# Kernel optimization log

Hardware: AMD Instinct MI355X
Metric: run time of the kernel (lower is better)

## Reference

```python
import jax, jax.numpy as jnp
import numpy as np

NE = 64        # num experts
H = 1024       # hidden_size
F = 2048       # ffn_hidden_size per expert
T = 16384      # total tokens


def setup_inputs() -> dict:
    key = jax.random.key(0)
    k1, k2, k3 = jax.random.split(key, 3)
    x = jax.random.normal(k1, (T, H), jnp.float32)
    w1 = jax.random.normal(k2, (NE, F, H), jnp.float32) * 0.02
    w2 = jax.random.normal(k3, (NE, F, H), jnp.float32) * 0.02
    # ragged token counts per expert, summing exactly to T
    rng = np.random.default_rng(0)
    sizes = rng.multinomial(T, np.ones(NE) / NE)
    tokens_per_expert = jnp.asarray(sizes, jnp.int32)
    return {"x": x, "w1": w1, "w2": w2, "tokens_per_expert": tokens_per_expert}


def _grouped_gmm(x, w, sizes, trans_b=False):
    # grouped GEMM: per-expert segment of x multiplied by that expert's weight.
    # sizes are concrete host ints (group boundaries are static), so we emit
    # one GEMM per expert with static slices, matching gg.ops.gmm semantics.
    offs = np.concatenate([[0], np.cumsum(sizes)]).astype(np.int64)
    outs = []
    for e in range(len(sizes)):
        xe = x[int(offs[e]):int(offs[e + 1])]          # [n_e, k]
        we = w[e].T if trans_b else w[e]               # [k, n]
        outs.append(xe @ we)
    return jnp.concatenate(outs, axis=0)


def reference(x, w1, w2, tokens_per_expert):
    sizes = np.asarray(tokens_per_expert)
    h = _grouped_gmm(x, w1, sizes, trans_b=True)       # [T, F]
    h = jax.nn.gelu(h, approximate=False)              # torch F.gelu (exact erf)
    return _grouped_gmm(h, w2, sizes, trans_b=False)   # [T, H]
```

## Files before the change

kernel.cpp:

```cpp
#include <hip/hip_runtime.h>
#include <hip/hip_bf16.h>

#define NE 64
#define HDIM 1024
#define FDIM 2048
#define TDIM 16384

typedef __attribute__((ext_vector_type(8))) short short8;
typedef __attribute__((ext_vector_type(4))) float f32x4;
typedef unsigned short u16;
typedef unsigned int u32;

struct IC0 { static constexpr int v = 0; };
struct IC1 { static constexpr int v = 1; };
template<int W> struct WN { static constexpr int v = W; };

__device__ __forceinline__ u16 f2bf(float f) {
  return __bfloat16_as_ushort(__float2bfloat16(f));
}
__device__ __forceinline__ u32 pk2(float a, float b) {
  return (u32)f2bf(a) | ((u32)f2bf(b) << 16);
}
template<int N> __device__ __forceinline__ void waitv() {
  if constexpr (N == 2)       asm volatile("s_waitcnt vmcnt(2)" ::: "memory");
  else if constexpr (N == 4)  asm volatile("s_waitcnt vmcnt(4)" ::: "memory");
  else if constexpr (N == 8)  asm volatile("s_waitcnt vmcnt(8)" ::: "memory");
  else if constexpr (N == 10) asm volatile("s_waitcnt vmcnt(10)" ::: "memory");
}
__device__ __forceinline__ void waitl() {
  asm volatile("s_waitcnt lgkmcnt(0)" ::: "memory");
}

__global__ void k_prep(const int* __restrict__ tpe, int4* __restrict__ map,
                       int* __restrict__ nblocks) {
  if (threadIdx.x != 0 || blockIdx.x != 0) return;
  int off = 0, nb = 0;
  for (int e = 0; e < NE; ++e) {
    int n = tpe[e];
    for (int r = 0; r < n; r += 256) {
      int re = (r + 256 < n) ? (r + 256) : n;
      map[nb++] = make_int4(e, off + r, off + re, 0);
    }
    off += n;
  }
  *nblocks = nb;
}

__global__ void k_conv(const float4* __restrict__ in, uint2* __restrict__ out, int n4) {
  int stride = gridDim.x * blockDim.x;
  for (int i = blockIdx.x * blockDim.x + threadIdx.x; i < n4; i += stride) {
    float4 v = in[i];
    uint2 o;
    o.x = pk2(v.x, v.y);
    o.y = pk2(v.z, v.w);
    out[i] = o;
  }
}

template<int K, int N, bool GELU, int BMODE, int NY>
__global__ __launch_bounds__(512) void k_gemm(
    const u16* __restrict__ A, const float* __restrict__ Bf, void* __restrict__ C,
    const int4* __restrict__ map, const int* __restrict__ nblocks)
{
  const int mblk = (int)blockIdx.x / NY;
  const int nblk = (int)blockIdx.x % NY;
  if (mblk >= *nblocks) return;
  const int4 mi = map[mblk];
  const int e = mi.x, row0 = mi.y, rowend = mi.z;
  const int n0 = nblk << 7;
  const int NT = K / 32;
  constexpr int LB = (BMODE == 1) ? 2 : 8;

  __shared__ __align__(16) u16 sa[3][8192];
  __shared__ __align__(16) u16 sb[2][128 * 40];

  const int tid = threadIdx.x;
  const int wid = tid >> 6, lane = tid & 63;
  const int wr = wid >> 1, wc = wid & 1;
  const int fr = lane & 15, fq = lane >> 4;

  f32x4 acc[4][4];
#pragma unroll
  for (int m = 0; m < 4; ++m)
#pragma unroll
    for (int n = 0; n < 4; ++n) acc[m][n] = (f32x4)0.f;

  const float* B = Bf + (size_t)e * ((size_t)N * K);

  float4 rb1[2][2];
  float  rb2[2][8];
  const int bn  = tid & 127;
  const int oct = tid >> 7;

  auto issueA = [&](int t, int buf) {
#pragma unroll
    for (int i = 0; i < 2; ++i) {
      int slot = i * 512 + tid;
      int r = slot >> 2, c = slot & 3;
      int cs = c ^ ((r >> 1) & 3);
      int row = row0 + r;
      row = row < TDIM ? row : TDIM - 1;
      const u16* g = A + (size_t)row * K + t * 32 + cs * 8;
      __builtin_amdgcn_global_load_lds(
          (const __attribute__((address_space(1))) u32*)g,
          (__attribute__((address_space(3))) u32*)(&sa[buf][i * 4096 + wid * 512]),
          16, 0, 0);
    }
  };
  auto loadB = [&](int t, auto ic) {
    constexpr int S = decltype(ic)::v;
    if constexpr (BMODE == 1) {
#pragma unroll
      for (int i = 0; i < 2; ++i) {
        int slot = i * 512 + tid;
        rb1[S][i] = *(const float4*)(B + (size_t)(n0 + (slot >> 3)) * K + t * 32 + (slot & 7) * 4);
      }
    } else {
      const float* src = B + (size_t)(t * 32 + oct * 8) * N + n0 + bn;
#pragma unroll
      for (int i = 0; i < 8; ++i) rb2[S][i] = src[(size_t)i * N];
    }
  };
  auto writeB = [&](int buf, auto ic) {
    constexpr int S = decltype(ic)::v;
    if constexpr (BMODE == 1) {
#pragma unroll
      for (int i = 0; i < 2; ++i) {
        int slot = i * 512 + tid;
        uint2 o;
        o.x = pk2(rb1[S][i].x, rb1[S][i].y);
        o.y = pk2(rb1[S][i].z, rb1[S][i].w);
        *(uint2*)(&sb[buf][(slot >> 3) * 40 + (slot & 7) * 4]) = o;
      }
    } else {
      uint4 c;
      c.x = pk2(rb2[S][0], rb2[S][1]); c.y = pk2(rb2[S][2], rb2[S][3]);
      c.z = pk2(rb2[S][4], rb2[S][5]); c.w = pk2(rb2[S][6], rb2[S][7]);
      *(uint4*)(&sb[buf][bn * 40 + oct * 8]) = c;
    }
  };

  auto body = [&](int t, auto icCur, auto wn) {
    waitv<decltype(wn)::v>();
    waitl();
    __builtin_amdgcn_s_barrier();
    const int cur3 = t % 3, curb = t & 1, nxtb = curb ^ 1;
    short8 av[4], bv[4];
#pragma unroll
    for (int m = 0; m < 4; ++m) {
      const int row = wr * 64 + m * 16 + fr;
      av[m] = *(const short8*)(&sa[cur3][row * 32 + (fq ^ ((row >> 1) & 3)) * 8]);
    }
#pragma unroll
    for (int n = 0; n < 4; ++n)
      bv[n] = *(const short8*)(&sb[curb][(wc * 64 + n * 16 + fr) * 40 + fq * 8]);
    issueA((t + 2 < NT) ? (t + 2) : (NT - 1), (t + 2) % 3);
    writeB(nxtb, icCur);
    loadB((t + 3 < NT) ? (t + 3) : (NT - 1), icCur);
#pragma unroll
    for (int m = 0; m < 4; ++m)
#pragma unroll
      for (int n = 0; n < 4; ++n)
        acc[m][n] = __builtin_amdgcn_mfma_f32_16x16x32_bf16(av[m], bv[n], acc[m][n], 0, 0, 0);
  };

  issueA(0, 0);
  loadB(0, IC0{});
  issueA(1, 1);
  loadB(1, IC1{});
  waitv<2 + LB>();
  writeB(0, IC0{});
  loadB(2, IC0{});

  body(0, IC1{}, WN<LB>{});
  body(1, IC0{}, WN<2 + LB>{});
  for (int t = 2; t < NT; t += 2) {
    body(t,     IC1{}, WN<2 + LB>{});
    body(t + 1, IC0{}, WN<2 + LB>{});
  }

#pragma unroll
  for (int m = 0; m < 4; ++m) {
    const int rb = row0 + wr * 64 + m * 16 + fq * 4;
#pragma unroll
    for (int n = 0; n < 4; ++n) {
      const int col = n0 + wc * 64 + n * 16 + fr;
#pragma unroll
      for (int j = 0; j < 4; ++j) {
        int r = rb + j;
        if (r < rowend) {
          float vv = acc[m][n][j];
          if constexpr (GELU) {
            vv = 0.5f * vv * (1.f + erff(vv * 0.70710678118654752f));
            ((u16*)C)[(size_t)r * N + col] = f2bf(vv);
          } else {
            ((float*)C)[(size_t)r * N + col] = vv;
          }
        }
      }
    }
  }
}

extern "C" void kernel_launch(void* const* d_in, const int* in_sizes, int n_in,
                              void* d_out, int out_size, void* d_ws, size_t ws_size,
                              hipStream_t stream) {
  const float* x  = (const float*)d_in[0];
  const float* w1 = (const float*)d_in[1];
  const float* w2 = (const float*)d_in[2];
  const int*  tpe = (const int*)d_in[3];

  char* ws = (char*)d_ws;
  int4* map     = (int4*)ws;
  int*  nblocks = (int*)(ws + 4096);
  u16*  xb      = (u16*)(ws + 8192);
  u16*  hb      = xb + (size_t)TDIM * HDIM;

  k_prep<<<1, 64, 0, stream>>>(tpe, map, nblocks);
  k_conv<<<2048, 256, 0, stream>>>((const float4*)x, (uint2*)xb, (TDIM * HDIM) / 4);
  k_gemm<HDIM, FDIM, true,  1, 16><<<128 * 16, 512, 0, stream>>>(
      xb, w1, (void*)hb, map, nblocks);
  k_gemm<FDIM, HDIM, false, 2, 8><<<128 * 8, 512, 0, stream>>>(
      hb, w2, d_out, map, nblocks);
}
```

Before: 470.9 us.

## Load fp32 W1 tiles directly into LDS via async global_load_lds

The first grouped GEMM is split into its own kernel, which now streams fp32 W1 tiles straight into a triple-buffered, XOR-swizzled LDS buffer with global_load_lds. The bf16 conversion happens at fragment-read time rather than going through registers and an LDS store. This is meant to remove the register staging and the extra LDS write pass for B, and to simplify the pipeline to a single wait per step. In exchange it uses more LDS per block and converts each B fragment again for every wave that reads it.

```diff
diff --git a/kernel.cpp b/kernel.cpp
--- a/kernel.cpp
+++ b/kernel.cpp
@@ -23,7 +23,6 @@
 }
 template<int N> __device__ __forceinline__ void waitv() {
   if constexpr (N == 2)       asm volatile("s_waitcnt vmcnt(2)" ::: "memory");
-  else if constexpr (N == 4)  asm volatile("s_waitcnt vmcnt(4)" ::: "memory");
   else if constexpr (N == 8)  asm volatile("s_waitcnt vmcnt(8)" ::: "memory");
   else if constexpr (N == 10) asm volatile("s_waitcnt vmcnt(10)" ::: "memory");
 }
@@ -57,9 +56,9 @@
   }
 }
 
-template<int K, int N, bool GELU, int BMODE, int NY>
-__global__ __launch_bounds__(512) void k_gemm(
-    const u16* __restrict__ A, const float* __restrict__ Bf, void* __restrict__ C,
+template<int K, int N, int NY>
+__global__ __launch_bounds__(512) void k_gemm1(
+    const u16* __restrict__ A, const float* __restrict__ Bf, u16* __restrict__ C,
     const int4* __restrict__ map, const int* __restrict__ nblocks)
 {
   const int mblk = (int)blockIdx.x / NY;
@@ -69,10 +68,9 @@
   const int e = mi.x, row0 = mi.y, rowend = mi.z;
   const int n0 = nblk << 7;
   const int NT = K / 32;
-  constexpr int LB = (BMODE == 1) ? 2 : 8;
-
-  __shared__ __align__(16) u16 sa[3][8192];
-  __shared__ __align__(16) u16 sb[2][128 * 40];
+
+  __shared__ __align__(16) u16   sa[2][8192];
+  __shared__ __align__(16) float sbf[3][4096];
 
   const int tid = threadIdx.x;
   const int wid = tid >> 6, lane = tid & 63;
@@ -86,11 +84,6 @@
     for (int n = 0; n < 4; ++n) acc[m][n] = (f32x4)0.f;
 
   const float* B = Bf + (size_t)e * ((size_t)N * K);
-
-  float4 rb1[2][2];
-  float  rb2[2][8];
-  const int bn  = tid & 127;
-  const int oct = tid >> 7;
 
   auto issueA = [&](int t, int buf) {
 #pragma unroll
@@ -107,37 +100,135 @@
           16, 0, 0);
     }
   };
+  auto issueB = [&](int t, int buf) {
+#pragma unroll
+    for (int i = 0; i < 2; ++i) {
+      int slot = i * 512 + tid;
+      int nn = slot >> 3, p = slot & 7;
+      int cs = p ^ (nn & 7);
+      const float* g = B + (size_t)(n0 + nn) * K + t * 32 + cs * 4;
+      __builtin_amdgcn_global_load_lds(
+          (const __attribute__((address_space(1))) u32*)g,
+          (__attribute__((address_space(3))) u32*)(&sbf[buf][i * 2048 + wid * 256]),
+          16, 0, 0);
+    }
+  };
+
+  auto body = [&](int t) {
+    waitv<2>();
+    __builtin_amdgcn_s_barrier();
+    const int curA = t & 1, curB = t % 3;
+    issueA((t + 1 < NT) ? (t + 1) : (NT - 1), curA ^ 1);
+    issueB((t + 2 < NT) ? (t + 2) : (NT - 1), (t + 2) % 3);
+    short8 av[4], bv[4];
+#pragma unroll
+    for (int m = 0; m < 4; ++m) {
+      const int row = wr * 64 + m * 16 + fr;
+      av[m] = *(const short8*)(&sa[curA][row * 32 + (fq ^ ((row >> 1) & 3)) * 8]);
+    }
+#pragma unroll
+    for (int n = 0; n < 4; ++n) {
+      const int nn = wc * 64 + n * 16 + fr;
+      const int swz = nn & 7;
+      float4 lo = *(const float4*)(&sbf[curB][nn * 32 + ((fq * 2 + 0) ^ swz) * 4]);
+      float4 hi = *(const float4*)(&sbf[curB][nn * 32 + ((fq * 2 + 1) ^ swz) * 4]);
+      union { short8 s; u32 u[4]; } bb;
+      bb.u[0] = pk2(lo.x, lo.y); bb.u[1] = pk2(lo.z, lo.w);
+      bb.u[2] = pk2(hi.x, hi.y); bb.u[3] = pk2(hi.z, hi.w);
+      bv[n] = bb.s;
+    }
+#pragma unroll
+    for (int m = 0; m < 4; ++m)
+#pragma unroll
+      for (int n = 0; n < 4; ++n)
+        acc[m][n] = __builtin_amdgcn_mfma_f32_16x16x32_bf16(av[m], bv[n], acc[m][n], 0, 0, 0);
+  };
+
+  issueA(0, 0);
+  issueB(0, 0);
+  issueB(1, 1);
+  for (int t = 0; t < NT; ++t) body(t);
+
+#pragma unroll
+  for (int m = 0; m < 4; ++m) {
+    const int rb = row0 + wr * 64 + m * 16 + fq * 4;
+#pragma unroll
+    for (int n = 0; n < 4; ++n) {
+      const int col = n0 + wc * 64 + n * 16 + fr;
+#pragma unroll
+      for (int j = 0; j < 4; ++j) {
+        int r = rb + j;
+        if (r < rowend) {
+          float vv = acc[m][n][j];
+          vv = 0.5f * vv * (1.f + erff(vv * 0.70710678118654752f));
+          C[(size_t)r * N + col] = f2bf(vv);
+        }
+      }
+    }
+  }
+}
+
+template<int K, int N, int NY>
+__global__ __launch_bounds__(512) void k_gemm2(
+    const u16* __restrict__ A, const float* __restrict__ Bf, float* __restrict__ C,
+    const int4* __restrict__ map, const int* __restrict__ nblocks)
+{
+  const int mblk = (int)blockIdx.x / NY;
+  const int nblk = (int)blockIdx.x % NY;
+  if (mblk >= *nblocks) return;
+  const int4 mi = map[mblk];
+  const int e = mi.x, row0 = mi.y, rowend = mi.z;
+  const int n0 = nblk << 7;
+  const int NT = K / 32;
+  constexpr int LB = 8;
+
+  __shared__ __align__(16) u16 sa[3][8192];
+  __shared__ __align__(16) u16 sb[2][128 * 40];
+
+  const int tid = threadIdx.x;
+  const int wid = tid >> 6, lane = tid & 63;
+  const int wr = wid >> 1, wc = wid & 1;
+  const int fr = lane & 15, fq = lane >> 4;
+
+  f32x4 acc[4][4];
+#pragma unroll
+  for (int m = 0; m < 4; ++m)
+#pragma unroll
+    for (int n = 0; n < 4; ++n) acc[m][n] = (f32x4)0.f;
+
+  const float* B = Bf + (size_t)e * ((size_t)N * K);
+
+  float rb2[2][8];
+  const int bn  = tid & 127;
+  const int oct = tid >> 7;
+
+  auto issueA = [&](int t, int buf) {
+#pragma unroll
+    for (int i = 0; i < 2; ++i) {
+      int slot = i * 512 + tid;
+      int r = slot >> 2, c = slot & 3;
+      int cs = c ^ ((r >> 1) & 3);
+      int row = row0 + r;
+      row = row < TDIM ? row : TDIM - 1;
+      const u16* g = A + (size_t)row * K + t * 32 + cs * 8;
+      __builtin_amdgcn_global_load_lds(
+          (const __attribute__((address_space(1))) u32*)g,
+          (__attribute__((address_space(3))) u32*)(&sa[buf][i * 4096 + wid * 512]),
+          16, 0, 0);
+    }
+  };
   auto loadB = [&](int t, auto ic) {
     constexpr int S = decltype(ic)::v;
-    if constexpr (BMODE == 1) {
-#pragma unroll
-      for (int i = 0; i < 2; ++i) {
-        int slot = i * 512 + tid;
-        rb1[S][i] = *(const float4*)(B + (size_t)(n0 + (slot >> 3)) * K + t * 32 + (slot & 7) * 4);
-      }
-    } else {
-      const float* src = B + (size_t)(t * 32 + oct * 8) * N + n0 + bn;
-#pragma unroll
-      for (int i = 0; i < 8; ++i) rb2[S][i] = src[(size_t)i * N];
-    }
+    const float* src = B + (size_t)(t * 32 + oct * 8) * N + n0 + bn;
+#pragma unroll
+    for (int i = 0; i < 8; ++i) rb2[S][i] = src[(size_t)i * N];
   };
   auto writeB = [&](int buf, auto ic) {
     constexpr int S = decltype(ic)::v;
-    if constexpr (BMODE == 1) {
-#pragma unroll
-      for (int i = 0; i < 2; ++i) {
-        int slot = i * 512 + tid;
-        uint2 o;
-        o.x = pk2(rb1[S][i].x, rb1[S][i].y);
-        o.y = pk2(rb1[S][i].z, rb1[S][i].w);
-        *(uint2*)(&sb[buf][(slot >> 3) * 40 + (slot & 7) * 4]) = o;
-      }
-    } else {
-      uint4 c;
-      c.x = pk2(rb2[S][0], rb2[S][1]); c.y = pk2(rb2[S][2], rb2[S][3]);
-      c.z = pk2(rb2[S][4], rb2[S][5]); c.w = pk2(rb2[S][6], rb2[S][7]);
-      *(uint4*)(&sb[buf][bn * 40 + oct * 8]) = c;
-    }
+    uint4 c;
+    c.x = pk2(rb2[S][0], rb2[S][1]); c.y = pk2(rb2[S][2], rb2[S][3]);
+    c.z = pk2(rb2[S][4], rb2[S][5]); c.w = pk2(rb2[S][6], rb2[S][7]);
+    *(uint4*)(&sb[buf][bn * 40 + oct * 8]) = c;
   };
 
   auto body = [&](int t, auto icCur, auto wn) {
@@ -188,15 +279,7 @@
 #pragma unroll
       for (int j = 0; j < 4; ++j) {
         int r = rb + j;
-        if (r < rowend) {
-          float vv = acc[m][n][j];
-          if constexpr (GELU) {
-            vv = 0.5f * vv * (1.f + erff(vv * 0.70710678118654752f));
-            ((u16*)C)[(size_t)r * N + col] = f2bf(vv);
-          } else {
-            ((float*)C)[(size_t)r * N + col] = vv;
-          }
-        }
+        if (r < rowend) C[(size_t)r * N + col] = acc[m][n][j];
       }
     }
   }
@@ -218,8 +301,8 @@
 
   k_prep<<<1, 64, 0, stream>>>(tpe, map, nblocks);
   k_conv<<<2048, 256, 0, stream>>>((const float4*)x, (uint2*)xb, (TDIM * HDIM) / 4);
-  k_gemm<HDIM, FDIM, true,  1, 16><<<128 * 16, 512, 0, stream>>>(
-      xb, w1, (void*)hb, map, nblocks);
-  k_gemm<FDIM, HDIM, false, 2, 8><<<128 * 8, 512, 0, stream>>>(
-      hb, w2, d_out, map, nblocks);
-}
+  k_gemm1<HDIM, FDIM, 16><<<128 * 16, 512, 0, stream>>>(
+      xb, w1, hb, map, nblocks);
+  k_gemm2<FDIM, HDIM, 8><<<128 * 8, 512, 0, stream>>>(
+      hb, w2, (float*)d_out, map, nblocks);
+}
```

Measured after the change: 472.4 us. Within noise of the previous version (+0.3%).
